# Kernel tuning notes

Hardware: AMD Instinct MI355X
Metric: run time of the kernel (lower is better)

Reference implementation:

```python
import jax, jax.numpy as jnp
import numpy as np

MARGIN = 1.0
N, D = 8192, 256
NUM_CLASSES = 32


def setup_inputs() -> dict:
    key = jax.random.key(0)
    k1, k2 = jax.random.split(key)
    embeddings = jax.random.normal(k1, (N, D), dtype=jnp.float32)
    labels = jax.random.randint(k2, (N,), 0, NUM_CLASSES, dtype=jnp.int64)
    return {"embeddings": embeddings, "labels": labels}


def reference(embeddings, labels):
    # L2-normalize rows (F.normalize p=2 dim=1); subsequent cosine similarity
    # of unit vectors is just their dot product -> plain [N, N] matmul.
    e = embeddings / jnp.linalg.norm(embeddings, axis=1, keepdims=True)
    sim = e @ e.T  # [N, N] cosine similarity matrix

    pos_mask = (labels[:, None] == labels[None, :])  # [N, N] bool
    pos_count = jnp.sum(pos_mask)
    neg_count = pos_mask.size - pos_count

    # Fused masked-mean reductions (no boolean gather / dynamic shapes).
    pos_term = jnp.where(pos_mask, (1.0 - sim) ** 2, 0.0)
    neg_term = jnp.where(pos_mask, 0.0, jax.nn.relu(sim - MARGIN) ** 2)
    positive_loss = jnp.sum(pos_term) / pos_count
    negative_loss = jnp.sum(neg_term) / neg_count
    return positive_loss + negative_loss
```

## Files before the change

kernel.cpp:

```cpp
#include <hip/hip_runtime.h>
#include <hip/hip_bf16.h>
#include <stdint.h>

#define N_ROWS 8192
#define DIM 256
#define NUM_CLASSES 32
#define PC 384
#define TPC 6
#define NBLK3 (NUM_CLASSES * TPC)

typedef __attribute__((ext_vector_type(4))) float f32x4;
typedef __attribute__((ext_vector_type(8))) short bf16x8;

static __device__ inline unsigned short f2bf(float f) {
  union { float f; unsigned u; } v; v.f = f;
  unsigned r = v.u + 0x7FFFu + ((v.u >> 16) & 1u);
  return (unsigned short)(r >> 16);
}

static __device__ inline void async_copy16(const void* g, void* l) {
  __builtin_amdgcn_global_load_lds(
      (const __attribute__((address_space(1))) unsigned int*)g,
      (__attribute__((address_space(3))) unsigned int*)l, 16, 0, 0);
}

__global__ __launch_bounds__(512)
void normalize_kernel(const float* __restrict__ emb, unsigned short* __restrict__ en) {
  const int row = blockIdx.x * 8 + (threadIdx.x >> 6);
  const int lane = threadIdx.x & 63;
  const float4 v = reinterpret_cast<const float4*>(emb + (size_t)row * DIM)[lane];
  float s = v.x * v.x + v.y * v.y + v.z * v.z + v.w * v.w;
  #pragma unroll
  for (int o = 32; o; o >>= 1) s += __shfl_xor(s, o);
  const float inv = 1.0f / sqrtf(s);
  ushort4 o4;
  o4.x = f2bf(v.x * inv);
  o4.y = f2bf(v.y * inv);
  o4.z = f2bf(v.z * inv);
  o4.w = f2bf(v.w * inv);
  reinterpret_cast<ushort4*>(en + (size_t)row * DIM)[lane] = o4;
}

__global__ __launch_bounds__(256)
void prep_kernel(const int* __restrict__ labels,
                 unsigned short* __restrict__ en,
                 unsigned short* __restrict__ rowlist,
                 int* __restrict__ cnt) {
  const int c = blockIdx.x;
  const int t = threadIdx.x;
  __shared__ int rk;
  if (t == 0) rk = 0;
  __syncthreads();
  const int4* lp = (const int4*)labels;
  #pragma unroll
  for (int g = 0; g < 8; ++g) {
    const int i = g * 256 + t;
    const int4 L = lp[i];
    if (L.x == c) { const int r = atomicAdd(&rk, 1); if (r < PC) rowlist[c * PC + r] = (unsigned short)(i * 4); }
    if (L.y == c) { const int r = atomicAdd(&rk, 1); if (r < PC) rowlist[c * PC + r] = (unsigned short)(i * 4 + 1); }
    if (L.z == c) { const int r = atomicAdd(&rk, 1); if (r < PC) rowlist[c * PC + r] = (unsigned short)(i * 4 + 2); }
    if (L.w == c) { const int r = atomicAdd(&rk, 1); if (r < PC) rowlist[c * PC + r] = (unsigned short)(i * 4 + 3); }
  }
  __syncthreads();
  const int nc = (rk < PC) ? rk : PC;
  if (t == 0) cnt[c] = nc;
  for (int i = nc + t; i < PC; i += 256)
    rowlist[c * PC + i] = (unsigned short)N_ROWS;
  if (c == 0 && t < 128) ((int*)(en + (size_t)N_ROWS * DIM))[t] = 0;
}

__global__ __launch_bounds__(256)
void class_sim_kernel(const unsigned short* __restrict__ en,
                      const unsigned short* __restrict__ rowlist,
                      const int* __restrict__ cnt,
                      float2* __restrict__ parts) {
  const int b = blockIdx.x;
  const int c = b / TPC, q = b - c * TPC;
  const int ti = (q < 3) ? 0 : (q < 5) ? 1 : 2;
  const int tj = (q < 3) ? q : (q < 5) ? (q - 2) : 2;
  const int t = threadIdx.x;
  const int nc = cnt[c];
  if (ti * 128 >= nc || tj * 128 >= nc) {
    if (t == 0) parts[b] = (float2){0.f, 0.f};
    return;
  }
  const bool diag = (ti == tj);

  __shared__ __align__(16) short lA[2][128 * 64];
  __shared__ __align__(16) short lB[2][128 * 64];
  __shared__ float red[8];

  const int lane = t & 63;
  const int wid = t >> 6;
  const int r15 = lane & 15;
  const int wm = (wid >> 1) * 64;
  const int wn = (wid & 1) * 64;

  int rA[4], rB[4];
  #pragma unroll
  for (int it = 0; it < 4; ++it) {
    rA[it] = rowlist[c * PC + ti * 128 + it * 32 + (t >> 3)];
    rB[it] = rowlist[c * PC + tj * 128 + it * 32 + (t >> 3)];
  }
  const int cb = (((t & 7) ^ ((t >> 3) & 7)) << 4);

  auto stage = [&](int buf, int kt) {
    const int kb = kt * 128;
    #pragma unroll
    for (int it = 0; it < 4; ++it) {
      const int x = (it * 256 + t) * 16;
      async_copy16((const char*)en + (size_t)rA[it] * 512 + kb + cb,
                   (char*)&lA[buf][0] + x);
      if (!diag)
        async_copy16((const char*)en + (size_t)rB[it] * 512 + kb + cb,
                     (char*)&lB[buf][0] + x);
    }
  };

  f32x4 accf[4][4];
  #pragma unroll
  for (int i = 0; i < 4; ++i)
    #pragma unroll
    for (int j = 0; j < 4; ++j) accf[i][j] = (f32x4){0.f, 0.f, 0.f, 0.f};

  stage(0, 0);
  __syncthreads();

  int cur = 0;
  #pragma unroll
  for (int kt = 0; kt < 4; ++kt) {
    if (kt < 3) stage(cur ^ 1, kt + 1);

    const char* abase = (const char*)&lA[cur][0];
    const char* bbase = diag ? abase : (const char*)&lB[cur][0];
    #pragma unroll
    for (int kk = 0; kk < 2; ++kk) {
      const int cbase = kk * 64 + ((lane >> 4) << 4);
      bf16x8 af[4], bf[4];
      #pragma unroll
      for (int mi = 0; mi < 4; ++mi) {
        const int row = wm + mi * 16 + r15;
        const int off = row * 128 + (cbase ^ ((row & 7) << 4));
        af[mi] = *(const bf16x8*)(abase + off);
      }
      #pragma unroll
      for (int ni = 0; ni < 4; ++ni) {
        const int row = wn + ni * 16 + r15;
        const int off = row * 128 + (cbase ^ ((row & 7) << 4));
        bf[ni] = *(const bf16x8*)(bbase + off);
      }
      #pragma unroll
      for (int mi = 0; mi < 4; ++mi)
        #pragma unroll
        for (int ni = 0; ni < 4; ++ni)
          accf[mi][ni] = __builtin_amdgcn_mfma_f32_16x16x32_bf16(
              af[mi], bf[ni], accf[mi][ni], 0, 0, 0);
    }

    if (kt < 3) { __syncthreads(); cur ^= 1; }
  }

  float s1 = 0.f, s2 = 0.f;
  #pragma unroll
  for (int mi = 0; mi < 4; ++mi)
    #pragma unroll
    for (int ni = 0; ni < 4; ++ni)
      #pragma unroll
      for (int j = 0; j < 4; ++j) {
        const float s = accf[mi][ni][j];
        s1 += s;
        s2 += s * s;
      }
  if (!diag) { s1 *= 2.f; s2 *= 2.f; }

  #pragma unroll
  for (int o = 32; o; o >>= 1) { s1 += __shfl_down(s1, o); s2 += __shfl_down(s2, o); }
  if (lane == 0) { red[wid * 2] = s1; red[wid * 2 + 1] = s2; }
  __syncthreads();
  if (t == 0) {
    float2 v;
    v.x = red[0] + red[2] + red[4] + red[6];
    v.y = red[1] + red[3] + red[5] + red[7];
    parts[b] = v;
  }
}

__global__ __launch_bounds__(256)
void finalize_kernel(const int* __restrict__ cnt,
                     const float2* __restrict__ parts,
                     float* __restrict__ out) {
  __shared__ float rps[4], rns[4];
  const int t = threadIdx.x;
  float s1 = 0.f, s2 = 0.f;
  if (t < NBLK3) { const float2 v = parts[t]; s1 = v.x; s2 = v.y; }
  #pragma unroll
  for (int o = 32; o; o >>= 1) { s1 += __shfl_down(s1, o); s2 += __shfl_down(s2, o); }
  if ((t & 63) == 0) { rps[t >> 6] = s1; rns[t >> 6] = s2; }
  __syncthreads();
  if (t == 0) {
    const float S1 = rps[0] + rps[1] + rps[2] + rps[3];
    const float S2 = rns[0] + rns[1] + rns[2] + rns[3];
    float P = 0.f;
    for (int c = 0; c < NUM_CLASSES; ++c) { const float n = (float)cnt[c]; P += n * n; }
    out[0] = (P - 2.f * S1 + S2) / P;
  }
}

extern "C" void kernel_launch(void* const* d_in, const int* in_sizes, int n_in,
                              void* d_out, int out_size, void* d_ws, size_t ws_size,
                              hipStream_t stream) {
  const float* emb = (const float*)d_in[0];
  const int* labels = (const int*)d_in[1];
  float* out = (float*)d_out;

  unsigned short* en = (unsigned short*)d_ws;
  char* p = (char*)d_ws + (size_t)(N_ROWS + 1) * DIM * 2;
  unsigned short* rowlist = (unsigned short*)p;
  p += NUM_CLASSES * PC * 2;
  int* cnt = (int*)p;
  p += NUM_CLASSES * 4;
  float2* parts = (float2*)p;

  normalize_kernel<<<N_ROWS / 8, 512, 0, stream>>>(emb, en);
  prep_kernel<<<NUM_CLASSES, 256, 0, stream>>>(labels, en, rowlist, cnt);
  class_sim_kernel<<<NBLK3, 256, 0, stream>>>(en, rowlist, cnt, parts);
  finalize_kernel<<<1, 256, 0, stream>>>(cnt, parts, out);
}
```

Before: 24.78 us.

## Load full K-depth tiles into LDS at once instead of double-buffered K pipeline

Replaces the 4-stage double-buffered K loop in the class similarity kernel with a single bulk async copy of the whole 128x256 bf16 tiles for A and B into LDS, followed by one barrier and a fully unrolled MFMA loop over K. This removes the per-stage barriers and issues all global loads up front. In exchange, LDS use per block grows to 128 KB, which limits occupancy to one block per CU and removes any overlap between loading and compute.

```diff
diff --git a/kernel.cpp b/kernel.cpp
--- a/kernel.cpp
+++ b/kernel.cpp
@@ -86,78 +86,63 @@
   }
   const bool diag = (ti == tj);
 
-  __shared__ __align__(16) short lA[2][128 * 64];
-  __shared__ __align__(16) short lB[2][128 * 64];
+  __shared__ __align__(16) short lA[128 * 256];
+  __shared__ __align__(16) short lB[128 * 256];
   __shared__ float red[8];
 
   const int lane = t & 63;
   const int wid = t >> 6;
   const int r15 = lane & 15;
+
+  const int rbase = t >> 5;
+  const int cb = ((t & 31) * 16) ^ (rbase << 4);
+
+  #pragma unroll
+  for (int it = 0; it < 16; ++it) {
+    const int trow = it * 8 + rbase;
+    const int x = (it * 256 + t) * 16;
+    const int gA = rowlist[c * PC + ti * 128 + trow];
+    async_copy16((const char*)en + (size_t)gA * 512 + cb, (char*)lA + x);
+    if (!diag) {
+      const int gB = rowlist[c * PC + tj * 128 + trow];
+      async_copy16((const char*)en + (size_t)gB * 512 + cb, (char*)lB + x);
+    }
+  }
+  __syncthreads();
+
   const int wm = (wid >> 1) * 64;
   const int wn = (wid & 1) * 64;
-
-  int rA[4], rB[4];
-  #pragma unroll
-  for (int it = 0; it < 4; ++it) {
-    rA[it] = rowlist[c * PC + ti * 128 + it * 32 + (t >> 3)];
-    rB[it] = rowlist[c * PC + tj * 128 + it * 32 + (t >> 3)];
-  }
-  const int cb = (((t & 7) ^ ((t >> 3) & 7)) << 4);
-
-  auto stage = [&](int buf, int kt) {
-    const int kb = kt * 128;
-    #pragma unroll
-    for (int it = 0; it < 4; ++it) {
-      const int x = (it * 256 + t) * 16;
-      async_copy16((const char*)en + (size_t)rA[it] * 512 + kb + cb,
-                   (char*)&lA[buf][0] + x);
-      if (!diag)
-        async_copy16((const char*)en + (size_t)rB[it] * 512 + kb + cb,
-                     (char*)&lB[buf][0] + x);
+  const int kq = (lane >> 4) << 4;
+  const int sw = (r15 & 7) << 4;
+  const char* abase = (const char*)lA;
+  const char* bbase = diag ? abase : (const char*)lB;
+
+  f32x4 accf[4][4];
+  #pragma unroll
+  for (int i = 0; i < 4; ++i)
+    #pragma unroll
+    for (int j = 0; j < 4; ++j) accf[i][j] = (f32x4){0.f, 0.f, 0.f, 0.f};
+
+  #pragma unroll
+  for (int kc = 0; kc < 8; ++kc) {
+    const int cbase = kc * 64 + kq;
+    bf16x8 af[4], bf[4];
+    #pragma unroll
+    for (int mi = 0; mi < 4; ++mi) {
+      const int row = wm + mi * 16 + r15;
+      af[mi] = *(const bf16x8*)(abase + row * 512 + (cbase ^ sw));
     }
-  };
-
-  f32x4 accf[4][4];
-  #pragma unroll
-  for (int i = 0; i < 4; ++i)
-    #pragma unroll
-    for (int j = 0; j < 4; ++j) accf[i][j] = (f32x4){0.f, 0.f, 0.f, 0.f};
-
-  stage(0, 0);
-  __syncthreads();
-
-  int cur = 0;
-  #pragma unroll
-  for (int kt = 0; kt < 4; ++kt) {
-    if (kt < 3) stage(cur ^ 1, kt + 1);
-
-    const char* abase = (const char*)&lA[cur][0];
-    const char* bbase = diag ? abase : (const char*)&lB[cur][0];
-    #pragma unroll
-    for (int kk = 0; kk < 2; ++kk) {
-      const int cbase = kk * 64 + ((lane >> 4) << 4);
-      bf16x8 af[4], bf[4];
+    #pragma unroll
+    for (int ni = 0; ni < 4; ++ni) {
+      const int row = wn + ni * 16 + r15;
+      bf[ni] = *(const bf16x8*)(bbase + row * 512 + (cbase ^ sw));
+    }
+    #pragma unroll
+    for (int mi = 0; mi < 4; ++mi)
       #pragma unroll
-      for (int mi = 0; mi < 4; ++mi) {
-        const int row = wm + mi * 16 + r15;
-        const int off = row * 128 + (cbase ^ ((row & 7) << 4));
-        af[mi] = *(const bf16x8*)(abase + off);
-      }
-      #pragma unroll
-      for (int ni = 0; ni < 4; ++ni) {
-        const int row = wn + ni * 16 + r15;
-        const int off = row * 128 + (cbase ^ ((row & 7) << 4));
-        bf[ni] = *(const bf16x8*)(bbase + off);
-      }
-      #pragma unroll
-      for (int mi = 0; mi < 4; ++mi)
-        #pragma unroll
-        for (int ni = 0; ni < 4; ++ni)
-          accf[mi][ni] = __builtin_amdgcn_mfma_f32_16x16x32_bf16(
-              af[mi], bf[ni], accf[mi][ni], 0, 0, 0);
-    }
-
-    if (kt < 3) { __syncthreads(); cur ^= 1; }
+      for (int ni = 0; ni < 4; ++ni)
+        accf[mi][ni] = __builtin_amdgcn_mfma_f32_16x16x32_bf16(
+            af[mi], bf[ni], accf[mi][ni], 0, 0, 0);
   }
 
   float s1 = 0.f, s2 = 0.f;
```

Result: slower. 30.48 us (+23.0%).
